# Optimization experiments

Measured on AMD Instinct MI355X. Metric: run time of the kernel, lower is better.

## Reference

```python
import jax, jax.numpy as jnp
import numpy as np

TEMPERATURE = 0.5


def setup_inputs() -> dict:
    key = jax.random.key(0)
    k1, k2 = jax.random.split(key)
    emb = jax.random.normal(k1, (16384, 128), dtype=jnp.float32)
    emb = emb / jnp.linalg.norm(emb, axis=1, keepdims=True)  # L2-normalized, per docstring
    labels = jax.random.randint(k2, (16384,), 0, 64, dtype=jnp.int64)
    return {"embeddings": emb, "partition_labels": labels}


def reference(embeddings, partition_labels):
    n = embeddings.shape[0]
    # [N, N] similarity matrix, scaled by temperature
    sim = jnp.matmul(embeddings, embeddings.T) / TEMPERATURE
    exp_sim = jnp.exp(sim)
    eye = jnp.eye(n, dtype=bool)
    pos_mask = (partition_labels[None, :] == partition_labels[:, None]) & ~eye
    # numerator: sum of exp over positives; denominator: sum over all k != i
    pos_sum = jnp.sum(jnp.where(pos_mask, exp_sim, 0.0), axis=1)
    all_sum = jnp.sum(jnp.where(~eye, exp_sim, 0.0), axis=1)
    valid = jnp.any(pos_mask, axis=1)
    loss_i = -(jnp.log(pos_sum) - jnp.log(all_sum))
    n_valid = jnp.sum(valid)
    total = jnp.sum(jnp.where(valid, loss_i, 0.0))
    return jnp.where(n_valid > 0, total / n_valid, 0.0)
```

## Files before the change

kernel.cpp:

```cpp
#include <hip/hip_runtime.h>

#define N_EMB 16384
#define DIM 128
#define NSPLIT 8
#define CPS (N_EMB / NSPLIT)
#define BN 128
#define NCT (CPS / BN)
#define NLAB 64

typedef __bf16 bf16x8 __attribute__((ext_vector_type(8)));
typedef float f32x4 __attribute__((ext_vector_type(4)));
typedef unsigned short us8 __attribute__((ext_vector_type(8)));
typedef unsigned int u32;

#define SCALE 2.8853900817779268f
#define LN2 0.6931471805599453f

__device__ inline float fast_exp2(float x) {
#if __has_builtin(__builtin_amdgcn_exp2f)
  return __builtin_amdgcn_exp2f(x);
#else
  return exp2f(x);
#endif
}
__device__ inline float fast_log2(float x) {
#if __has_builtin(__builtin_amdgcn_logf)
  return __builtin_amdgcn_logf(x);
#else
  return log2f(x);
#endif
}

__device__ inline unsigned short f2bf(float f) {
  unsigned int u = __float_as_uint(f);
  u += 0x7fffu + ((u >> 16) & 1u);
  return (unsigned short)(u >> 16);
}

__device__ inline void gll16(const unsigned short* g, unsigned short* l) {
  __builtin_amdgcn_global_load_lds(
      (const __attribute__((address_space(1))) u32*)g,
      (__attribute__((address_space(3))) u32*)l, 16, 0, 0);
}

__global__ __launch_bounds__(1024) void perm_kernel(
    const int* __restrict__ labels, int* __restrict__ perm,
    int* __restrict__ gstart) {
  __shared__ int hist[NLAB];
  __shared__ int cur[NLAB];
  const int tid = threadIdx.x;
  if (tid < NLAB) hist[tid] = 0;
  __syncthreads();
  for (int i = tid; i < N_EMB; i += 1024) atomicAdd(&hist[labels[i]], 1);
  __syncthreads();
  if (tid == 0) {
    int s = 0;
    for (int l = 0; l < NLAB; ++l) {
      gstart[l] = s;
      cur[l] = s;
      s += hist[l];
    }
    gstart[NLAB] = s;
  }
  __syncthreads();
  for (int i = tid; i < N_EMB; i += 1024) {
    int p = atomicAdd(&cur[labels[i]], 1);
    perm[p] = i;
  }
}

__global__ __launch_bounds__(256) void preconv(
    const float* __restrict__ emb, const int* __restrict__ perm,
    unsigned short* __restrict__ eraw, unsigned short* __restrict__ escal) {
  const int tid = threadIdx.x;
  const int tile = blockIdx.x >> 2;
  const int part = blockIdx.x & 3;
  const size_t base = (size_t)tile * (128 * DIM);
#pragma unroll
  for (int i = 0; i < 2; ++i) {
    int G = part * 512 + i * 256 + tid;
    int col16 = G & 15;
    int qd = (G >> 4) & 3;
    int ks = (G >> 6) & 3;
    int tc = G >> 8;
    int srow = perm[tile * 128 + tc * 16 + col16];
    const float* p = emb + (size_t)srow * DIM + ks * 32 + qd * 8;
    float4 a = *reinterpret_cast<const float4*>(p);
    float4 b = *reinterpret_cast<const float4*>(p + 4);
    us8 g, s;
    g[0] = f2bf(a.x); g[1] = f2bf(a.y); g[2] = f2bf(a.z); g[3] = f2bf(a.w);
    g[4] = f2bf(b.x); g[5] = f2bf(b.y); g[6] = f2bf(b.z); g[7] = f2bf(b.w);
#pragma unroll
    for (int j = 0; j < 8; ++j) {
      float f = __uint_as_float((u32)g[j] << 16) * SCALE;
      s[j] = f2bf(f);
    }
    *reinterpret_cast<us8*>(eraw + base + (size_t)G * 8) = g;
    *reinterpret_cast<us8*>(escal + base + (size_t)G * 8) = s;
  }
}

__global__ __launch_bounds__(128, 2) void cl_all(
    const unsigned short* __restrict__ eraw,
    const unsigned short* __restrict__ escal, float* __restrict__ ws_all) {
  __shared__ unsigned short lds[BN * DIM];
  const int tid = threadIdx.x;
  const int lane = tid & 63;
  const int w = tid >> 6;
  const int col16 = lane & 15;
  const int quad = lane >> 4;
  const int r0 = blockIdx.x * 128;
  const int cs = blockIdx.y;

  bf16x8 afrag[4][4];
#pragma unroll
  for (int tr = 0; tr < 4; ++tr) {
    const int T = (r0 >> 4) + w * 4 + tr;
    const unsigned short* p = escal + (size_t)(T >> 3) * (128 * DIM) +
                              ((T & 7) * 4) * 512 + lane * 8;
#pragma unroll
    for (int ks = 0; ks < 4; ++ks)
      afrag[tr][ks] = *reinterpret_cast<const bf16x8*>(p + ks * 512);
  }

  float all_p[16];
#pragma unroll
  for (int t = 0; t < 16; ++t) all_p[t] = 0.f;

  for (int ct = 0; ct < NCT; ++ct) {
    const int c0 = cs * CPS + ct * BN;
    __syncthreads();
    {
      const unsigned short* g = eraw + (size_t)c0 * DIM;
#pragma unroll
      for (int i = 0; i < 16; ++i) {
        int chunk = i * 2 + w;
        gll16(g + chunk * 512 + lane * 8, lds + chunk * 512);
      }
    }
    __syncthreads();

#pragma unroll
    for (int tc = 0; tc < 8; ++tc) {
      bf16x8 bfr[4];
#pragma unroll
      for (int ks = 0; ks < 4; ++ks)
        bfr[ks] = *reinterpret_cast<const bf16x8*>(lds + (tc * 4 + ks) * 512 +
                                                   lane * 8);
#pragma unroll
      for (int tr = 0; tr < 4; ++tr) {
        f32x4 acc = {0.f, 0.f, 0.f, 0.f};
#pragma unroll
        for (int ks = 0; ks < 4; ++ks)
          acc = __builtin_amdgcn_mfma_f32_16x16x32_bf16(afrag[tr][ks], bfr[ks],
                                                        acc, 0, 0, 0);
#pragma unroll
        for (int r = 0; r < 4; ++r)
          all_p[tr * 4 + r] += fast_exp2(acc[r]);
      }
    }
  }

#pragma unroll
  for (int t = 0; t < 16; ++t) {
    float a = all_p[t];
#pragma unroll
    for (int m = 8; m >= 1; m >>= 1) a += __shfl_xor(a, m, 64);
    if (col16 == 0) {
      int row_g = r0 + w * 64 + (t >> 2) * 16 + quad * 4 + (t & 3);
      ws_all[cs * N_EMB + row_g] = a;
    }
  }
}

__global__ __launch_bounds__(256) void cl_pos(
    const unsigned short* __restrict__ eraw,
    const unsigned short* __restrict__ escal, const int* __restrict__ gstart,
    float* __restrict__ ws_pos, float* __restrict__ ws_diag) {
  const int l = blockIdx.x;
  const int chunk = blockIdx.y;
  const int gs = gstart[l], ge = gstart[l + 1];
  const int tid = threadIdx.x;
  const int lane = tid & 63;
  const int w = tid >> 6;
  const int col16 = lane & 15;
  const int quad = lane >> 4;
  const int t0 = gs >> 4;
  const int t1 = (ge + 15) >> 4;

  for (int ta = t0 + chunk * 4 + w; ta < t1; ta += 16) {
    bf16x8 af[4];
    const unsigned short* pa = escal + (size_t)(ta >> 3) * (128 * DIM) +
                               ((ta & 7) * 4) * 512 + lane * 8;
#pragma unroll
    for (int ks = 0; ks < 4; ++ks)
      af[ks] = *reinterpret_cast<const bf16x8*>(pa + ks * 512);
    const int grow = ta * 16 + quad * 4;
    float posr[4] = {0.f, 0.f, 0.f, 0.f};

    for (int tb = t0; tb < t1; ++tb) {
      bf16x8 bfr[4];
      const unsigned short* pb = eraw + (size_t)(tb >> 3) * (128 * DIM) +
                                 ((tb & 7) * 4) * 512 + lane * 8;
#pragma unroll
      for (int ks = 0; ks < 4; ++ks)
        bfr[ks] = *reinterpret_cast<const bf16x8*>(pb + ks * 512);
      f32x4 acc = {0.f, 0.f, 0.f, 0.f};
#pragma unroll
      for (int ks = 0; ks < 4; ++ks)
        acc = __builtin_amdgcn_mfma_f32_16x16x32_bf16(af[ks], bfr[ks], acc, 0,
                                                      0, 0);
      const int gcol = tb * 16 + col16;
      const bool colin = (gcol >= gs) && (gcol < ge);
#pragma unroll
      for (int r = 0; r < 4; ++r) {
        float e = fast_exp2(acc[r]);
        const int gr = grow + r;
        if (gcol == gr) {
          if (colin) ws_diag[gr] = e;
        } else if (colin) {
          posr[r] += e;
        }
      }
    }

#pragma unroll
    for (int r = 0; r < 4; ++r) {
      float p = posr[r];
#pragma unroll
      for (int m = 8; m >= 1; m >>= 1) p += __shfl_xor(p, m, 64);
      const int gr = grow + r;
      if (col16 == 0 && gr >= gs && gr < ge) ws_pos[gr] = p;
    }
  }
}

__global__ __launch_bounds__(256) void fin1(
    const float* __restrict__ ws_all, const float* __restrict__ ws_pos,
    const float* __restrict__ ws_diag, float* __restrict__ part_tot,
    int* __restrict__ part_cnt) {
  __shared__ float s_t[256];
  __shared__ int s_c[256];
  const int tid = threadIdx.x;
  const int row = blockIdx.x * 256 + tid;
  float a = 0.f;
#pragma unroll
  for (int s = 0; s < NSPLIT; ++s) a += ws_all[s * N_EMB + row];
  a -= ws_diag[row];
  const float p = ws_pos[row];
  float t = 0.f;
  int c = 0;
  if (p > 0.f) {
    t = fast_log2(a) - fast_log2(p);
    c = 1;
  }
  s_t[tid] = t;
  s_c[tid] = c;
  __syncthreads();
  for (int s = 128; s > 0; s >>= 1) {
    if (tid < s) {
      s_t[tid] += s_t[tid + s];
      s_c[tid] += s_c[tid + s];
    }
    __syncthreads();
  }
  if (tid == 0) {
    part_tot[blockIdx.x] = s_t[0];
    part_cnt[blockIdx.x] = s_c[0];
  }
}

__global__ __launch_bounds__(64) void fin2(const float* __restrict__ part_tot,
                                           const int* __restrict__ part_cnt,
                                           float* __restrict__ out) {
  const int tid = threadIdx.x;
  float t = part_tot[tid];
  int c = part_cnt[tid];
#pragma unroll
  for (int m = 32; m >= 1; m >>= 1) {
    t += __shfl_xor(t, m, 64);
    c += __shfl_xor(c, m, 64);
  }
  if (tid == 0) out[0] = (c > 0) ? (t * LN2 / (float)c) : 0.f;
}

extern "C" void kernel_launch(void* const* d_in, const int* in_sizes, int n_in,
                              void* d_out, int out_size, void* d_ws,
                              size_t ws_size, hipStream_t stream) {
  const float* emb = (const float*)d_in[0];
  const int* labels = (const int*)d_in[1];

  unsigned short* eraw = (unsigned short*)d_ws;
  unsigned short* escal = eraw + (size_t)N_EMB * DIM;
  float* ws_all = (float*)(escal + (size_t)N_EMB * DIM);
  float* ws_pos = ws_all + NSPLIT * N_EMB;
  float* ws_diag = ws_pos + N_EMB;
  float* part_tot = ws_diag + N_EMB;
  int* part_cnt = (int*)(part_tot + 64);
  int* perm = part_cnt + 64;
  int* gstart = perm + N_EMB;

  perm_kernel<<<1, 1024, 0, stream>>>(labels, perm, gstart);
  preconv<<<512, 256, 0, stream>>>(emb, perm, eraw, escal);
  cl_all<<<dim3(N_EMB / 128, NSPLIT), 128, 0, stream>>>(eraw, escal, ws_all);
  cl_pos<<<dim3(NLAB, 4), 256, 0, stream>>>(eraw, escal, gstart, ws_pos,
                                            ws_diag);
  fin1<<<N_EMB / 256, 256, 0, stream>>>(ws_all, ws_pos, ws_diag, part_tot,
                                        part_cnt);
  fin2<<<1, 64, 0, stream>>>(part_tot, part_cnt, (float*)d_out);
}
```

Measured before the change: 169.0 us.

## Widen cl_all blocks to share LDS tiles, scale on load, per-wave histogram perm

Measured after the change: 415.8 us. 146% more time.

```diff
diff --git a/kernel.cpp b/kernel.cpp
--- a/kernel.cpp
+++ b/kernel.cpp
@@ -2,7 +2,7 @@
 
 #define N_EMB 16384
 #define DIM 128
-#define NSPLIT 8
+#define NSPLIT 16
 #define CPS (N_EMB / NSPLIT)
 #define BN 128
 #define NCT (CPS / BN)
@@ -46,32 +46,56 @@
 __global__ __launch_bounds__(1024) void perm_kernel(
     const int* __restrict__ labels, int* __restrict__ perm,
     int* __restrict__ gstart) {
-  __shared__ int hist[NLAB];
-  __shared__ int cur[NLAB];
-  const int tid = threadIdx.x;
-  if (tid < NLAB) hist[tid] = 0;
-  __syncthreads();
-  for (int i = tid; i < N_EMB; i += 1024) atomicAdd(&hist[labels[i]], 1);
+  __shared__ int whist[16][NLAB];
+  __shared__ int htot[NLAB];
+  const int tid = threadIdx.x;
+  const int w = tid >> 6, lane = tid & 63;
+  whist[w][lane] = 0;
+  __syncthreads();
+  const int base_i = w * 1024;
+  int mylab[16];
+#pragma unroll
+  for (int k = 0; k < 16; ++k) {
+    int lab = labels[base_i + k * 64 + lane];
+    mylab[k] = lab;
+    atomicAdd(&whist[w][lab], 1);
+  }
+  __syncthreads();
+  if (tid < NLAB) {
+    int s = 0;
+#pragma unroll
+    for (int ww = 0; ww < 16; ++ww) {
+      int t = whist[ww][tid];
+      whist[ww][tid] = s;
+      s += t;
+    }
+    htot[tid] = s;
+  }
   __syncthreads();
   if (tid == 0) {
     int s = 0;
     for (int l = 0; l < NLAB; ++l) {
+      int t = htot[l];
       gstart[l] = s;
-      cur[l] = s;
-      s += hist[l];
+      htot[l] = s;
+      s += t;
     }
     gstart[NLAB] = s;
   }
   __syncthreads();
-  for (int i = tid; i < N_EMB; i += 1024) {
-    int p = atomicAdd(&cur[labels[i]], 1);
-    perm[p] = i;
+  whist[w][lane] += htot[lane];
+  __syncthreads();
+#pragma unroll
+  for (int k = 0; k < 16; ++k) {
+    int lab = mylab[k];
+    int pos = atomicAdd(&whist[w][lab], 1);
+    perm[pos] = base_i + k * 64 + lane;
   }
 }
 
 __global__ __launch_bounds__(256) void preconv(
     const float* __restrict__ emb, const int* __restrict__ perm,
-    unsigned short* __restrict__ eraw, unsigned short* __restrict__ escal) {
+    unsigned short* __restrict__ eraw) {
   const int tid = threadIdx.x;
   const int tile = blockIdx.x >> 2;
   const int part = blockIdx.x & 3;
@@ -87,40 +111,41 @@
     const float* p = emb + (size_t)srow * DIM + ks * 32 + qd * 8;
     float4 a = *reinterpret_cast<const float4*>(p);
     float4 b = *reinterpret_cast<const float4*>(p + 4);
-    us8 g, s;
+    us8 g;
     g[0] = f2bf(a.x); g[1] = f2bf(a.y); g[2] = f2bf(a.z); g[3] = f2bf(a.w);
     g[4] = f2bf(b.x); g[5] = f2bf(b.y); g[6] = f2bf(b.z); g[7] = f2bf(b.w);
-#pragma unroll
-    for (int j = 0; j < 8; ++j) {
-      float f = __uint_as_float((u32)g[j] << 16) * SCALE;
-      s[j] = f2bf(f);
-    }
     *reinterpret_cast<us8*>(eraw + base + (size_t)G * 8) = g;
-    *reinterpret_cast<us8*>(escal + base + (size_t)G * 8) = s;
-  }
-}
-
-__global__ __launch_bounds__(128, 2) void cl_all(
-    const unsigned short* __restrict__ eraw,
-    const unsigned short* __restrict__ escal, float* __restrict__ ws_all) {
+  }
+}
+
+__device__ inline bf16x8 load_scaled(const unsigned short* p) {
+  us8 v = *reinterpret_cast<const us8*>(p);
+  us8 s;
+#pragma unroll
+  for (int j = 0; j < 8; ++j)
+    s[j] = f2bf(__uint_as_float((u32)v[j] << 16) * SCALE);
+  return *reinterpret_cast<bf16x8*>(&s);
+}
+
+__global__ __launch_bounds__(256, 4) void cl_all(
+    const unsigned short* __restrict__ eraw, float* __restrict__ ws_all) {
   __shared__ unsigned short lds[BN * DIM];
   const int tid = threadIdx.x;
   const int lane = tid & 63;
   const int w = tid >> 6;
   const int col16 = lane & 15;
   const int quad = lane >> 4;
-  const int r0 = blockIdx.x * 128;
+  const int r0 = blockIdx.x * 256;
   const int cs = blockIdx.y;
 
   bf16x8 afrag[4][4];
 #pragma unroll
   for (int tr = 0; tr < 4; ++tr) {
     const int T = (r0 >> 4) + w * 4 + tr;
-    const unsigned short* p = escal + (size_t)(T >> 3) * (128 * DIM) +
+    const unsigned short* p = eraw + (size_t)(T >> 3) * (128 * DIM) +
                               ((T & 7) * 4) * 512 + lane * 8;
 #pragma unroll
-    for (int ks = 0; ks < 4; ++ks)
-      afrag[tr][ks] = *reinterpret_cast<const bf16x8*>(p + ks * 512);
+    for (int ks = 0; ks < 4; ++ks) afrag[tr][ks] = load_scaled(p + ks * 512);
   }
 
   float all_p[16];
@@ -133,8 +158,8 @@
     {
       const unsigned short* g = eraw + (size_t)c0 * DIM;
 #pragma unroll
-      for (int i = 0; i < 16; ++i) {
-        int chunk = i * 2 + w;
+      for (int i = 0; i < 8; ++i) {
+        int chunk = i * 4 + w;
         gll16(g + chunk * 512 + lane * 8, lds + chunk * 512);
       }
     }
@@ -155,8 +180,7 @@
           acc = __builtin_amdgcn_mfma_f32_16x16x32_bf16(afrag[tr][ks], bfr[ks],
                                                         acc, 0, 0, 0);
 #pragma unroll
-        for (int r = 0; r < 4; ++r)
-          all_p[tr * 4 + r] += fast_exp2(acc[r]);
+        for (int r = 0; r < 4; ++r) all_p[tr * 4 + r] += fast_exp2(acc[r]);
       }
     }
   }
@@ -174,8 +198,7 @@
 }
 
 __global__ __launch_bounds__(256) void cl_pos(
-    const unsigned short* __restrict__ eraw,
-    const unsigned short* __restrict__ escal, const int* __restrict__ gstart,
+    const unsigned short* __restrict__ eraw, const int* __restrict__ gstart,
     float* __restrict__ ws_pos, float* __restrict__ ws_diag) {
   const int l = blockIdx.x;
   const int chunk = blockIdx.y;
@@ -190,11 +213,10 @@
 
   for (int ta = t0 + chunk * 4 + w; ta < t1; ta += 16) {
     bf16x8 af[4];
-    const unsigned short* pa = escal + (size_t)(ta >> 3) * (128 * DIM) +
+    const unsigned short* pa = eraw + (size_t)(ta >> 3) * (128 * DIM) +
                                ((ta & 7) * 4) * 512 + lane * 8;
 #pragma unroll
-    for (int ks = 0; ks < 4; ++ks)
-      af[ks] = *reinterpret_cast<const bf16x8*>(pa + ks * 512);
+    for (int ks = 0; ks < 4; ++ks) af[ks] = load_scaled(pa + ks * 512);
     const int grow = ta * 16 + quad * 4;
     float posr[4] = {0.f, 0.f, 0.f, 0.f};
 
@@ -291,8 +313,7 @@
   const int* labels = (const int*)d_in[1];
 
   unsigned short* eraw = (unsigned short*)d_ws;
-  unsigned short* escal = eraw + (size_t)N_EMB * DIM;
-  float* ws_all = (float*)(escal + (size_t)N_EMB * DIM);
+  float* ws_all = (float*)(eraw + (size_t)N_EMB * DIM);
   float* ws_pos = ws_all + NSPLIT * N_EMB;
   float* ws_diag = ws_pos + N_EMB;
   float* part_tot = ws_diag + N_EMB;
@@ -301,10 +322,9 @@
   int* gstart = perm + N_EMB;
 
   perm_kernel<<<1, 1024, 0, stream>>>(labels, perm, gstart);
-  preconv<<<512, 256, 0, stream>>>(emb, perm, eraw, escal);
-  cl_all<<<dim3(N_EMB / 128, NSPLIT), 128, 0, stream>>>(eraw, escal, ws_all);
-  cl_pos<<<dim3(NLAB, 4), 256, 0, stream>>>(eraw, escal, gstart, ws_pos,
-                                            ws_diag);
+  preconv<<<512, 256, 0, stream>>>(emb, perm, eraw);
+  cl_all<<<dim3(N_EMB / 256, NSPLIT), 256, 0, stream>>>(eraw, ws_all);
+  cl_pos<<<dim3(NLAB, 4), 256, 0, stream>>>(eraw, gstart, ws_pos, ws_diag);
   fin1<<<N_EMB / 256, 256, 0, stream>>>(ws_all, ws_pos, ws_diag, part_tot,
                                         part_cnt);
   fin2<<<1, 64, 0, stream>>>(part_tot, part_cnt, (float*)d_out);
```
